# Performance work log

Measured on AMD Instinct MI355X. Metric: run time of the kernel, lower is better.

## Reference

```python
import jax, jax.numpy as jnp
import numpy as np

D_MODEL = 1024
NEG_INF = -1e9


def setup_inputs() -> dict:
    key = jax.random.key(0)
    ks = jax.random.split(key, 9)
    B, S, D = 8, 2048, D_MODEL
    q = jax.random.normal(ks[0], (B, S, D), dtype=jnp.float32)
    k = jax.random.normal(ks[1], (B, S, D), dtype=jnp.float32)
    v = jax.random.normal(ks[2], (B, S, D), dtype=jnp.float32)
    mask = jax.random.randint(ks[3], (B, S), 0, 2, dtype=jnp.int32)
    scale = 1.0 / np.sqrt(D)
    Wq = jax.random.normal(ks[4], (D, D), dtype=jnp.float32) * scale
    bq = jnp.zeros((D,), dtype=jnp.float32)
    Wout = jax.random.normal(ks[5], (D, D), dtype=jnp.float32) * scale
    bout = jnp.zeros((D,), dtype=jnp.float32)
    return {"q": q, "k": k, "v": v, "mask": mask,
            "Wq": Wq, "bq": bq, "Wout": Wout, "bout": bout}


def reference(q, k, v, mask, Wq, bq, Wout, bout):
    # Faithful to original: the SAME q_linear projects q, k and v.
    qp = jnp.einsum('bsd,ed->bse', q, Wq) + bq
    kp = jnp.einsum('bsd,ed->bse', k, Wq) + bq
    vp = jnp.einsum('bsd,ed->bse', v, Wq) + bq
    d_k = q.shape[-1]
    # original divides K by sqrt(d_k) before the matmul (same math as scaling scores)
    scores = jnp.einsum('bqd,bkd->bqk', qp, kp) / jnp.sqrt(jnp.float32(d_k))  # [B,Sq,Sk]
    m = mask[:, None, :]  # [B,1,Sk]
    scores = jnp.where(m == 0, jnp.float32(-1e9), scores)
    weights = jax.nn.softmax(scores, axis=-1)
    out = jnp.einsum('bqk,bkd->bqd', weights, vp)
    out = jnp.einsum('bqd,ed->bqe', out, Wout) + bout
    return (out, weights)
```

## Files before the change

### kernel.cpp

```cpp
#include <hip/hip_runtime.h>
#include <hip/hip_bf16.h>

typedef __attribute__((ext_vector_type(8))) short short8;
typedef __attribute__((ext_vector_type(4))) float f32x4;

#define S_LEN 2048
#define DM 1024
#define NBATCH 8

__device__ __forceinline__ ushort f2b(float f) {
    union { float f; unsigned u; } a; a.f = f;
    unsigned u = a.u;
    u += 0x7fffu + ((u >> 16) & 1u);
    return (ushort)(u >> 16);
}

__device__ __forceinline__ unsigned pkbf(float a, float b) {
    float2 t; t.x = a; t.y = b;
    __hip_bfloat162 h = __float22bfloat162_rn(t);
    union { __hip_bfloat162 h; unsigned u; } c; c.h = h;
    return c.u;
}

#define GLDS(gp, lp) __builtin_amdgcn_global_load_lds( \
    (const __attribute__((address_space(1))) void*)(gp), \
    (__attribute__((address_space(3))) void*)(lp), 16, 0, 0)

template<int OMODE, bool HAS_BIAS>
__global__ __launch_bounds__(512, 2) void gemm256(
    const ushort* __restrict__ A, const ushort* __restrict__ B,
    void* __restrict__ Cv, const float* __restrict__ bias,
    int K, int lda, int ldb, int ldc,
    long long sA, long long sB, long long sC)
{
    __shared__ __align__(16) ushort lA[2][256 * 64];
    __shared__ __align__(16) ushort lB[2][256 * 64];

    const int t = threadIdx.x;
    const int lane = t & 63;
    const int wid = t >> 6;
    const int wm = wid >> 2, wn = wid & 3;
    const int z = blockIdx.z;

    const int gx = gridDim.x, gy = gridDim.y;
    const int nwg = gx * gy;
    const int lid = blockIdx.y * gx + blockIdx.x;
    const int qq = nwg >> 3, r8 = nwg & 7;
    const int xcd = lid & 7, off = lid >> 3;
    const int w = (xcd < r8 ? xcd * (qq + 1) : r8 * (qq + 1) + (xcd - r8) * qq) + off;
    const int bm = w / gy, bn = w % gy;

    const ushort* Ap = A + (size_t)z * sA + (size_t)(bm * 256) * lda;
    const ushort* Bp = B + (size_t)z * sB + (size_t)(bn * 256) * ldb;

    f32x4 acc[8][4] = {};

    const int srow = t >> 3;
    const int scol = (((t & 7) ^ (srow & 7))) * 8;
    const int nK = K >> 6;

    const int r = lane & 15;
    const int swz = (r & 7) << 4;

    auto stage = [&](int kt, int buf) {
        const int k0 = kt * 64;
        const ushort* ga = Ap + (size_t)srow * lda + k0 + scol;
        char* dA = (char*)lA[buf];
#pragma unroll
        for (int i = 0; i < 4; i++)
            GLDS(ga + (size_t)(64 * i) * lda, dA + i * 8192 + t * 16);
        const ushort* gb = Bp + (size_t)srow * ldb + k0 + scol;
        char* dB = (char*)lB[buf];
#pragma unroll
        for (int i = 0; i < 4; i++)
            GLDS(gb + (size_t)(64 * i) * ldb, dB + i * 8192 + t * 16);
    };

    stage(0, 0);
    __syncthreads();

    int cur = 0;
    for (int kt = 0; kt < nK; ++kt) {
        if (kt + 1 < nK) stage(kt + 1, cur ^ 1);
        const char* la = (const char*)lA[cur];
        const char* lb = (const char*)lB[cur];
#pragma unroll
        for (int mh = 0; mh < 2; mh++) {
            short8 af[4][2];
#pragma unroll
            for (int m = 0; m < 4; m++) {
                const int row = wm * 128 + mh * 64 + m * 16 + r;
#pragma unroll
                for (int ks = 0; ks < 2; ks++)
                    af[m][ks] = *(const short8*)(la + row * 128 + ((ks * 64 + (lane >> 4) * 16) ^ swz));
            }
#pragma unroll
            for (int nh = 0; nh < 2; nh++) {
                short8 bf[2][2];
#pragma unroll
                for (int n = 0; n < 2; n++) {
                    const int row = wn * 64 + nh * 32 + n * 16 + r;
#pragma unroll
                    for (int ks = 0; ks < 2; ks++)
                        bf[n][ks] = *(const short8*)(lb + row * 128 + ((ks * 64 + (lane >> 4) * 16) ^ swz));
                }
                __builtin_amdgcn_s_setprio(1);
#pragma unroll
                for (int m = 0; m < 4; m++)
#pragma unroll
                    for (int n = 0; n < 2; n++)
#pragma unroll
                        for (int ks = 0; ks < 2; ks++)
                            acc[mh * 4 + m][nh * 2 + n] = __builtin_amdgcn_mfma_f32_16x16x32_bf16(
                                af[m][ks], bf[n][ks], acc[mh * 4 + m][nh * 2 + n], 0, 0, 0);
                __builtin_amdgcn_s_setprio(0);
            }
        }
        __syncthreads();
        cur ^= 1;
    }

    const int ro = (lane >> 4) * 4;
    const int colb = bn * 256 + wn * 64;
    const int rowb = bm * 256 + wm * 128;
    float bv[4];
    if constexpr (HAS_BIAS) {
#pragma unroll
        for (int n = 0; n < 4; n++) bv[n] = bias[colb + n * 16 + r];
    }

    if constexpr (OMODE == 0) {
        float* Cp = (float*)Cv + (size_t)z * sC;
#pragma unroll
        for (int m = 0; m < 8; m++)
#pragma unroll
            for (int n = 0; n < 4; n++) {
                const int col = colb + n * 16 + r;
#pragma unroll
                for (int j = 0; j < 4; j++) {
                    float vv = acc[m][n][j];
                    if constexpr (HAS_BIAS) vv += bv[n];
                    Cp[(size_t)(rowb + m * 16 + ro + j) * ldc + col] = vv;
                }
            }
    } else if constexpr (OMODE == 1) {
        ushort* Cp = (ushort*)Cv + (size_t)z * sC;
#pragma unroll
        for (int m = 0; m < 8; m++)
#pragma unroll
            for (int n = 0; n < 4; n++) {
                const int col = colb + n * 16 + r;
#pragma unroll
                for (int j = 0; j < 4; j++) {
                    float vv = acc[m][n][j];
                    if constexpr (HAS_BIAS) vv += bv[n];
                    Cp[(size_t)(rowb + m * 16 + ro + j) * ldc + col] = f2b(vv);
                }
            }
    } else {
        ushort* Cp = (ushort*)Cv + (size_t)z * sC;
#pragma unroll
        for (int m = 0; m < 8; m++)
#pragma unroll
            for (int n = 0; n < 4; n++) {
                const int col = colb + n * 16 + r;
                float v0 = acc[m][n][0], v1 = acc[m][n][1], v2 = acc[m][n][2], v3 = acc[m][n][3];
                if constexpr (HAS_BIAS) { v0 += bv[n]; v1 += bv[n]; v2 += bv[n]; v3 += bv[n]; }
                ushort4 u;
                u.x = f2b(v0); u.y = f2b(v1); u.z = f2b(v2); u.w = f2b(v3);
                *(ushort4*)&Cp[(size_t)col * ldc + rowb + m * 16 + ro] = u;
            }
    }
}

__global__ __launch_bounds__(256) void cast_f32_bf16_k(
    const float* __restrict__ in, ushort* __restrict__ outp, int n)
{
    int idx = (blockIdx.x * 256 + threadIdx.x) * 4;
    if (idx >= n) return;
    float4 f = *(const float4*)&in[idx];
    uint2 u; u.x = pkbf(f.x, f.y); u.y = pkbf(f.z, f.w);
    *(uint2*)&outp[idx] = u;
}

__global__ __launch_bounds__(256) void cast3_k(
    const float* __restrict__ q, const float* __restrict__ k,
    const float* __restrict__ v, ushort* __restrict__ outp, int n_each)
{
    const float* src = (blockIdx.y == 0) ? q : (blockIdx.y == 1) ? k : v;
    ushort* dst = outp + (size_t)blockIdx.y * n_each;
    const int stride = gridDim.x * 256 * 4;
    for (int idx = (blockIdx.x * 256 + threadIdx.x) * 4; idx < n_each; idx += stride) {
        float4 f = *(const float4*)&src[idx];
        uint2 u; u.x = pkbf(f.x, f.y); u.y = pkbf(f.z, f.w);
        *(uint2*)&dst[idx] = u;
    }
}

__global__ __launch_bounds__(256) void softmax_rows(
    float* __restrict__ w, const int* __restrict__ mask, ushort* __restrict__ wb)
{
    __shared__ float red[8];
    const int rid = blockIdx.x;
    const int b = rid >> 11;
    float* row = w + (size_t)rid * S_LEN;
    ushort* brow = wb + (size_t)rid * S_LEN;
    const int* mrow = mask + (size_t)b * S_LEN;
    const int t = threadIdx.x;
    const int wid = t >> 6, lane = t & 63;
    const float scale = 0.03125f;

    float x[8];
    float mx = -3.0e38f;
#pragma unroll
    for (int i = 0; i < 2; i++) {
        const int idx = (t + i * 256) * 4;
        float4 s4 = *(const float4*)&row[idx];
        int4 m4 = *(const int4*)&mrow[idx];
        float* xp = &x[i * 4];
        xp[0] = (m4.x == 0) ? -1.0e9f : s4.x * scale;
        xp[1] = (m4.y == 0) ? -1.0e9f : s4.y * scale;
        xp[2] = (m4.z == 0) ? -1.0e9f : s4.z * scale;
        xp[3] = (m4.w == 0) ? -1.0e9f : s4.w * scale;
        mx = fmaxf(mx, fmaxf(fmaxf(xp[0], xp[1]), fmaxf(xp[2], xp[3])));
    }
#pragma unroll
    for (int off = 32; off; off >>= 1) mx = fmaxf(mx, __shfl_xor(mx, off));
    if (lane == 0) red[wid] = mx;
    __syncthreads();
    mx = fmaxf(fmaxf(red[0], red[1]), fmaxf(red[2], red[3]));

    float sum = 0.0f;
#pragma unroll
    for (int i = 0; i < 8; i++) { x[i] = __expf(x[i] - mx); sum += x[i]; }
#pragma unroll
    for (int off = 32; off; off >>= 1) sum += __shfl_xor(sum, off);
    if (lane == 0) red[4 + wid] = sum;
    __syncthreads();
    sum = red[4] + red[5] + red[6] + red[7];
    const float inv = 1.0f / sum;

#pragma unroll
    for (int i = 0; i < 2; i++) {
        const int idx = (t + i * 256) * 4;
        float4 o;
        o.x = x[i * 4 + 0] * inv; o.y = x[i * 4 + 1] * inv;
        o.z = x[i * 4 + 2] * inv; o.w = x[i * 4 + 3] * inv;
        *(float4*)&row[idx] = o;
        uint2 ub;
        ub.x = pkbf(o.x, o.y);
        ub.y = pkbf(o.z, o.w);
        *(uint2*)&brow[idx] = ub;
    }
}

extern "C" void kernel_launch(void* const* d_in, const int* in_sizes, int n_in,
                              void* d_out, int out_size, void* d_ws, size_t ws_size,
                              hipStream_t stream)
{
    const float* q    = (const float*)d_in[0];
    const float* k    = (const float*)d_in[1];
    const float* v    = (const float*)d_in[2];
    const int*   mask = (const int*)d_in[3];
    const float* Wq   = (const float*)d_in[4];
    const float* bq   = (const float*)d_in[5];
    const float* Wout = (const float*)d_in[6];
    const float* bout = (const float*)d_in[7];

    float* out     = (float*)d_out;
    float* weights = out + (size_t)NBATCH * S_LEN * DM;

    const size_t NTOK = (size_t)NBATCH * S_LEN;

    ushort* qkvb = (ushort*)weights;
    ushort* qb = qkvb;
    ushort* kb = qb + NTOK * DM;
    ushort* vb = kb + NTOK * DM;
    ushort* wbf = (ushort*)d_out;

    ushort* qp    = (ushort*)d_ws;
    ushort* kp    = qp + NTOK * DM;
    ushort* vpT   = kp + NTOK * DM;
    ushort* attn  = qp;
    ushort* Wqb   = vpT + NTOK * DM;
    ushort* Woutb = Wqb + (size_t)DM * DM;

    dim3 blk(256, 1, 1);
    dim3 blk5(512, 1, 1);

    cast_f32_bf16_k<<<dim3(1024, 1, 1), blk, 0, stream>>>(Wq, Wqb, DM * DM);
    cast_f32_bf16_k<<<dim3(1024, 1, 1), blk, 0, stream>>>(Wout, Woutb, DM * DM);
    cast3_k<<<dim3(2048, 3, 1), blk, 0, stream>>>(q, k, v, qkvb, (int)(NTOK * DM));

    gemm256<1, true><<<dim3(64, 4, 1), blk5, 0, stream>>>(
        qb, Wqb, qp, bq, 1024, 1024, 1024, 1024, 0, 0, 0);
    gemm256<1, true><<<dim3(64, 4, 1), blk5, 0, stream>>>(
        kb, Wqb, kp, bq, 1024, 1024, 1024, 1024, 0, 0, 0);
    gemm256<2, true><<<dim3(8, 4, NBATCH), blk5, 0, stream>>>(
        vb, Wqb, vpT, bq, 1024, 1024, 1024, 2048,
        (long long)S_LEN * DM, 0, (long long)DM * S_LEN);

    gemm256<0, false><<<dim3(8, 8, NBATCH), blk5, 0, stream>>>(
        qp, kp, weights, nullptr, 1024, 1024, 1024, 2048,
        (long long)S_LEN * DM, (long long)S_LEN * DM, (long long)S_LEN * S_LEN);

    softmax_rows<<<dim3(NBATCH * S_LEN, 1, 1), blk, 0, stream>>>(weights, mask, wbf);

    gemm256<1, false><<<dim3(8, 4, NBATCH), blk5, 0, stream>>>(
        wbf, vpT, attn, nullptr, 2048, 2048, 2048, 1024,
        (long long)S_LEN * S_LEN, (long long)DM * S_LEN, (long long)S_LEN * DM);

    gemm256<0, true><<<dim3(64, 4, 1), blk5, 0, stream>>>(
        attn, Woutb, out, bout, 1024, 1024, 1024, 1024, 0, 0, 0);
}
```

Measured before the change: 472.2 us.

## Split GEMM LDS tiles into halves and interleave loads with MFMA quadrants

Splits the 256x64 LDS tiles of the bf16 GEMM into two 128-row halves per operand. Each k-iteration is restructured into four MFMA quadrants, and each half-tile load for kt+1 or kt+2 is issued between them, with explicit vmcnt waits and raw s_barrier calls. B fragments are reused across both M halves, so fewer LDS reads are needed per iteration. The goal is a deeper, finer-grained prefetch that hides global-to-LDS latency behind compute. The cost is many more barriers per iteration and fragile hand-managed wait counts.

```diff
diff --git a/kernel.cpp b/kernel.cpp
--- a/kernel.cpp
+++ b/kernel.cpp
@@ -25,6 +25,19 @@
 #define GLDS(gp, lp) __builtin_amdgcn_global_load_lds( \
     (const __attribute__((address_space(1))) void*)(gp), \
     (__attribute__((address_space(3))) void*)(lp), 16, 0, 0)
+
+#define BAR() __builtin_amdgcn_s_barrier()
+#define VMW(N) asm volatile("s_waitcnt vmcnt(" #N ")" ::: "memory")
+
+#define QUAD(AF, BF, MH, NH) do {                                              \
+    __builtin_amdgcn_s_setprio(1);                                             \
+    _Pragma("unroll") for (int m_ = 0; m_ < 4; m_++)                           \
+    _Pragma("unroll") for (int n_ = 0; n_ < 2; n_++)                           \
+    _Pragma("unroll") for (int ks_ = 0; ks_ < 2; ks_++)                        \
+        acc[(MH)*4 + m_][(NH)*2 + n_] = __builtin_amdgcn_mfma_f32_16x16x32_bf16( \
+            AF[m_][ks_], BF[n_][ks_], acc[(MH)*4 + m_][(NH)*2 + n_], 0, 0, 0); \
+    __builtin_amdgcn_s_setprio(0);                                             \
+} while (0)
 
 template<int OMODE, bool HAS_BIAS>
 __global__ __launch_bounds__(512, 2) void gemm256(
@@ -33,8 +46,8 @@
     int K, int lda, int ldb, int ldc,
     long long sA, long long sB, long long sC)
 {
-    __shared__ __align__(16) ushort lA[2][256 * 64];
-    __shared__ __align__(16) ushort lB[2][256 * 64];
+    __shared__ __align__(16) ushort lA[2][2][128 * 64];
+    __shared__ __align__(16) ushort lB[2][2][128 * 64];
 
     const int t = threadIdx.x;
     const int lane = t & 63;
@@ -56,67 +69,93 @@
     f32x4 acc[8][4] = {};
 
     const int srow = t >> 3;
-    const int scol = (((t & 7) ^ (srow & 7))) * 8;
+    const int scol = ((t & 7) ^ (srow & 7)) * 8;
+
+    auto stA = [&](int kt, int h, int buf) {
+        const ushort* g = Ap + (size_t)(h * 128 + srow) * lda + kt * 64 + scol;
+        char* d = (char*)lA[buf][h];
+        GLDS(g, d + t * 16);
+        GLDS(g + (size_t)64 * lda, d + 8192 + t * 16);
+    };
+    auto stB = [&](int kt, int h, int buf) {
+        const ushort* g = Bp + (size_t)(h * 128 + srow) * ldb + kt * 64 + scol;
+        char* d = (char*)lB[buf][h];
+        GLDS(g, d + t * 16);
+        GLDS(g + (size_t)64 * ldb, d + 8192 + t * 16);
+    };
+
     const int nK = K >> 6;
+
+    stA(0, 0, 0); stB(0, 0, 0); stA(0, 1, 0); stB(0, 1, 0);
+    if (nK > 1) {
+        stA(1, 0, 1); stB(1, 0, 1);
+        VMW(4);
+    } else {
+        VMW(0);
+    }
+    BAR();
 
     const int r = lane & 15;
     const int swz = (r & 7) << 4;
-
-    auto stage = [&](int kt, int buf) {
-        const int k0 = kt * 64;
-        const ushort* ga = Ap + (size_t)srow * lda + k0 + scol;
-        char* dA = (char*)lA[buf];
-#pragma unroll
-        for (int i = 0; i < 4; i++)
-            GLDS(ga + (size_t)(64 * i) * lda, dA + i * 8192 + t * 16);
-        const ushort* gb = Bp + (size_t)srow * ldb + k0 + scol;
-        char* dB = (char*)lB[buf];
-#pragma unroll
-        for (int i = 0; i < 4; i++)
-            GLDS(gb + (size_t)(64 * i) * ldb, dB + i * 8192 + t * 16);
-    };
-
-    stage(0, 0);
-    __syncthreads();
+    const int cb0 = ((lane >> 4) * 16) ^ swz;
+    const int cb1 = (64 + (lane >> 4) * 16) ^ swz;
+    const int lbr = (wn & 1) * 64;
+    const int bh = wn >> 1;
 
     int cur = 0;
     for (int kt = 0; kt < nK; ++kt) {
-        if (kt + 1 < nK) stage(kt + 1, cur ^ 1);
-        const char* la = (const char*)lA[cur];
-        const char* lb = (const char*)lB[cur];
-#pragma unroll
-        for (int mh = 0; mh < 2; mh++) {
-            short8 af[4][2];
-#pragma unroll
-            for (int m = 0; m < 4; m++) {
-                const int row = wm * 128 + mh * 64 + m * 16 + r;
-#pragma unroll
-                for (int ks = 0; ks < 2; ks++)
-                    af[m][ks] = *(const short8*)(la + row * 128 + ((ks * 64 + (lane >> 4) * 16) ^ swz));
-            }
-#pragma unroll
-            for (int nh = 0; nh < 2; nh++) {
-                short8 bf[2][2];
-#pragma unroll
-                for (int n = 0; n < 2; n++) {
-                    const int row = wn * 64 + nh * 32 + n * 16 + r;
-#pragma unroll
-                    for (int ks = 0; ks < 2; ks++)
-                        bf[n][ks] = *(const short8*)(lb + row * 128 + ((ks * 64 + (lane >> 4) * 16) ^ swz));
-                }
-                __builtin_amdgcn_s_setprio(1);
-#pragma unroll
-                for (int m = 0; m < 4; m++)
-#pragma unroll
-                    for (int n = 0; n < 2; n++)
-#pragma unroll
-                        for (int ks = 0; ks < 2; ks++)
-                            acc[mh * 4 + m][nh * 2 + n] = __builtin_amdgcn_mfma_f32_16x16x32_bf16(
-                                af[m][ks], bf[n][ks], acc[mh * 4 + m][nh * 2 + n], 0, 0, 0);
-                __builtin_amdgcn_s_setprio(0);
-            }
-        }
-        __syncthreads();
+        const char* la = (const char*)lA[cur][wm];
+        const char* lb = (const char*)lB[cur][bh];
+        short8 af[4][2], b0f[2][2], b1f[2][2];
+
+#pragma unroll
+        for (int m = 0; m < 4; m++) {
+            const int lr = m * 16 + r;
+            af[m][0] = *(const short8*)(la + lr * 128 + cb0);
+            af[m][1] = *(const short8*)(la + lr * 128 + cb1);
+        }
+#pragma unroll
+        for (int n = 0; n < 2; n++) {
+            const int lr = lbr + n * 16 + r;
+            b0f[n][0] = *(const short8*)(lb + lr * 128 + cb0);
+            b0f[n][1] = *(const short8*)(lb + lr * 128 + cb1);
+        }
+        if (kt + 1 < nK) stA(kt + 1, 1, cur ^ 1);
+        BAR();
+        QUAD(af, b0f, 0, 0);
+        BAR();
+
+#pragma unroll
+        for (int n = 0; n < 2; n++) {
+            const int lr = lbr + 32 + n * 16 + r;
+            b1f[n][0] = *(const short8*)(lb + lr * 128 + cb0);
+            b1f[n][1] = *(const short8*)(lb + lr * 128 + cb1);
+        }
+        if (kt + 1 < nK) stB(kt + 1, 1, cur ^ 1);
+        BAR();
+        QUAD(af, b1f, 0, 1);
+        BAR();
+
+#pragma unroll
+        for (int m = 0; m < 4; m++) {
+            const int lr = 64 + m * 16 + r;
+            af[m][0] = *(const short8*)(la + lr * 128 + cb0);
+            af[m][1] = *(const short8*)(la + lr * 128 + cb1);
+        }
+        if (kt + 2 < nK) stB(kt + 2, 0, cur);
+        BAR();
+        QUAD(af, b0f, 1, 0);
+        BAR();
+
+        if (kt + 2 < nK) stA(kt + 2, 0, cur);
+        BAR();
+        QUAD(af, b1f, 1, 1);
+        BAR();
+
+        if (kt + 1 < nK) {
+            if (kt + 1 == nK - 1) { VMW(0); } else { VMW(4); }
+            BAR();
+        }
         cur ^= 1;
     }
 
```

After: 458.0 us. 3.0% less time.
